# Performance work log

Measured on AMD Instinct MI355X. Metric: run time of the kernel, lower is better.

Reference implementation:

```python
import jax, jax.numpy as jnp
import numpy as np

N_MODES, BATCH, PH, PW = 4, 1024, 128, 128
OBJ_C, OBJ_H, OBJ_W = 1, 2048, 2048


def setup_inputs() -> dict:
    key = jax.random.key(0)
    k1, k2, k3 = jax.random.split(key, 3)
    obj = jax.random.normal(k1, (OBJ_C, OBJ_H, OBJ_W), dtype=jnp.float32)
    waves = jax.random.normal(k2, (N_MODES, BATCH, PH, PW), dtype=jnp.float32)
    pos = jax.random.randint(k3, (BATCH, 2), 0, OBJ_H - PH, dtype=jnp.int32)
    return {"obj": obj, "waves": waves, "pos": pos}


def reference(obj, waves, pos):
    B, H, W = waves.shape[1], waves.shape[2], waves.shape[3]
    # patch_norm = sum over probe modes of |waves|^2  -> [B, H, W]
    patch_norm = jnp.sum(waves * waves, axis=0)
    # overlap_intensity: scatter-add each patch into object_norm at its corner pos
    rows = pos[:, 0, None] + jnp.arange(H)          # [B, H]
    cols = pos[:, 1, None] + jnp.arange(W)          # [B, W]
    object_norm = jnp.zeros(obj.shape[1:], jnp.float32).at[
        rows[:, :, None], cols[:, None, :]
    ].add(patch_norm)
    # batch_crop: gather object patches at each position -> [B, C, H, W]
    C = obj.shape[0]
    def crop_one(p):
        return jax.lax.dynamic_slice(obj, (0, p[0], p[1]), (C, H, W))
    patches = jax.vmap(crop_one)(pos)
    return patches, object_norm
```

## Files before the change

kernel.cpp:

```cpp
#include <hip/hip_runtime.h>


#define NMODES 4
#define NB     1024
#define PH     128
#define PW     128
#define OH     2048
#define OW     2048

#define TS       32
#define NT_X     (OW / TS)
#define NT_Y     (OH / TS)
#define NT       (NT_X * NT_Y)
#define CAP      64
#define UNROLL   4

__global__ __launch_bounds__(256) void crop_and_bin(
    const float* __restrict__ obj,
    const int*   __restrict__ pos,
    float* __restrict__ patches,
    int*   __restrict__ tile_cnt,
    int*   __restrict__ tile_list)
{
    const int q = blockIdx.x * blockDim.x + threadIdx.x;

    if (q < NB) {
        const int r0 = pos[2 * q];
        const int c0 = pos[2 * q + 1];
        const int ty0 = r0 >> 5, ty1 = (r0 + PH - 1) >> 5;
        const int tx0 = c0 >> 5, tx1 = (c0 + PW - 1) >> 5;
        for (int ty = ty0; ty <= ty1; ++ty)
            for (int tx = tx0; tx <= tx1; ++tx) {
                const int t = ty * NT_X + tx;
                const int idx = atomicAdd(&tile_cnt[t], 1);
                if (idx < CAP) tile_list[t * CAP + idx] = q;
            }
    }

    const int b     = q >> 12;
    const int local = q & 4095;
    const int h     = local >> 5;
    const int w     = (local & 31) << 2;

    const int r0 = pos[b * 2 + 0];
    const int c0 = pos[b * 2 + 1];

    const int oidx = (r0 + h) * OW + (c0 + w);
    float4 p;
    p.x = obj[oidx + 0];
    p.y = obj[oidx + 1];
    p.z = obj[oidx + 2];
    p.w = obj[oidx + 3];
    *reinterpret_cast<float4*>(patches + b * (PH * PW) + h * PW + w) = p;
}

__global__ __launch_bounds__(256) void norm_gather(
    const float* __restrict__ waves,
    const int*   __restrict__ pos,
    const int*   __restrict__ tile_cnt,
    const int*   __restrict__ tile_list,
    float* __restrict__ norm)
{
    const int t  = blockIdx.x;
    const int Y0 = (t >> 6) * TS;
    const int X0 = (t & 63) * TS;

    __shared__ int s_base[CAP + UNROLL];
    __shared__ int s_r[CAP + UNROLL];
    __shared__ int s_c[CAP + UNROLL];

    const int count = min(tile_cnt[t], CAP);
    const int cpad  = (count + UNROLL - 1) & ~(UNROLL - 1);
    for (int i = threadIdx.x; i < cpad; i += 256) {
        if (i < count) {
            const int b = tile_list[t * CAP + i];
            s_base[i] = b * (PH * PW);
            s_r[i]    = pos[2 * b];
            s_c[i]    = pos[2 * b + 1];
        } else {
            s_base[i] = 0;
            s_r[i]    = 1 << 20;
            s_c[i]    = 1 << 20;
        }
    }
    __syncthreads();

    const int x     = threadIdx.x & 31;
    const int phase = threadIdx.x >> 5;
    const int X     = X0 + x;
    const int Y     = Y0 + phase;

    const int MS = NB * PH * PW;

    float acc0 = 0.0f, acc1 = 0.0f, acc2 = 0.0f, acc3 = 0.0f;

    #pragma unroll 2
    for (int i = 0; i < cpad; ++i) {
        const int r0 = s_r[i];
        const int c0 = s_c[i];
        const int bb = s_base[i];

        const int dc  = X - c0;
        const bool vc = (unsigned)dc < (unsigned)PW;
        const int dcc = min(max(dc, 0), PW - 1);

        const int dr0 = Y      - r0;
        const int dr1 = Y + 8  - r0;
        const int dr2 = Y + 16 - r0;
        const int dr3 = Y + 24 - r0;

        const bool v0 = vc & ((unsigned)dr0 < (unsigned)PH);
        const bool v1 = vc & ((unsigned)dr1 < (unsigned)PH);
        const bool v2 = vc & ((unsigned)dr2 < (unsigned)PH);
        const bool v3 = vc & ((unsigned)dr3 < (unsigned)PH);

        const int drc0 = min(max(dr0, 0), PH - 1);
        const int drc1 = min(max(dr1, 0), PH - 1);
        const int drc2 = min(max(dr2, 0), PH - 1);
        const int drc3 = min(max(dr3, 0), PH - 1);

        const float* w0p = waves + bb + drc0 * PW + dcc;
        const float* w1p = waves + bb + drc1 * PW + dcc;
        const float* w2p = waves + bb + drc2 * PW + dcc;
        const float* w3p = waves + bb + drc3 * PW + dcc;

        const float a0 = w0p[0], a1 = w0p[MS], a2 = w0p[2 * MS], a3 = w0p[3 * MS];
        const float b0 = w1p[0], b1 = w1p[MS], b2 = w1p[2 * MS], b3 = w1p[3 * MS];
        const float c0f = w2p[0], c1 = w2p[MS], c2 = w2p[2 * MS], c3 = w2p[3 * MS];
        const float d0 = w3p[0], d1 = w3p[MS], d2 = w3p[2 * MS], d3 = w3p[3 * MS];

        const float s0 = a0 * a0 + a1 * a1 + a2 * a2 + a3 * a3;
        const float s1 = b0 * b0 + b1 * b1 + b2 * b2 + b3 * b3;
        const float s2 = c0f * c0f + c1 * c1 + c2 * c2 + c3 * c3;
        const float s3 = d0 * d0 + d1 * d1 + d2 * d2 + d3 * d3;

        acc0 += v0 ? s0 : 0.0f;
        acc1 += v1 ? s1 : 0.0f;
        acc2 += v2 ? s2 : 0.0f;
        acc3 += v3 ? s3 : 0.0f;
    }

    norm[(Y     ) * OW + X] = acc0;
    norm[(Y +  8) * OW + X] = acc1;
    norm[(Y + 16) * OW + X] = acc2;
    norm[(Y + 24) * OW + X] = acc3;
}

extern "C" void kernel_launch(void* const* d_in, const int* in_sizes, int n_in,
                              void* d_out, int out_size, void* d_ws, size_t ws_size,
                              hipStream_t stream) {
    const float* obj   = (const float*)d_in[0];
    const float* waves = (const float*)d_in[1];
    const int*   pos   = (const int*)d_in[2];

    float* patches = (float*)d_out;
    float* norm    = (float*)d_out + (size_t)NB * PH * PW;

    int* tile_cnt  = (int*)d_ws;
    int* tile_list = tile_cnt + NT;

    hipMemsetAsync(tile_cnt, 0, NT * sizeof(int), stream);

    const int quads = NB * PH * PW / 4;
    crop_and_bin<<<quads / 256, 256, 0, stream>>>(obj, pos, patches,
                                                  tile_cnt, tile_list);
    norm_gather<<<NT, 256, 0, stream>>>(waves, pos, tile_cnt,
                                        tile_list, norm);
}
```

Before: 430.1 us.

## Use 128-wide bins sliced into 8-row blocks with row-overlap skip

Enlarges the binning tiles from 32x32 to 128x128, which cuts the per-patch atomic bin insertions from up to 25 to up to 4. Each bin is now processed by 16 blocks of 8 rows by 128 columns, so each warp reads full 128-float patch rows. Each block skips patches whose rows do not overlap its slice. Each block scans a longer candidate list, and lanes outside a patch's columns still issue clamped loads. The CAP of 64 per bin is more likely to overflow with larger tiles.

```diff
diff --git a/kernel.cpp b/kernel.cpp
--- a/kernel.cpp
+++ b/kernel.cpp
@@ -8,12 +8,13 @@
 #define OH     2048
 #define OW     2048
 
-#define TS       32
+#define TS       128
 #define NT_X     (OW / TS)
 #define NT_Y     (OH / TS)
 #define NT       (NT_X * NT_Y)
 #define CAP      64
-#define UNROLL   4
+#define SLICES   16
+#define SH       (TS / SLICES)
 
 __global__ __launch_bounds__(256) void crop_and_bin(
     const float* __restrict__ obj,
@@ -27,8 +28,8 @@
     if (q < NB) {
         const int r0 = pos[2 * q];
         const int c0 = pos[2 * q + 1];
-        const int ty0 = r0 >> 5, ty1 = (r0 + PH - 1) >> 5;
-        const int tx0 = c0 >> 5, tx1 = (c0 + PW - 1) >> 5;
+        const int ty0 = r0 >> 7, ty1 = (r0 + PH - 1) >> 7;
+        const int tx0 = c0 >> 7, tx1 = (c0 + PW - 1) >> 7;
         for (int ty = ty0; ty <= ty1; ++ty)
             for (int tx = tx0; tx <= tx1; ++tx) {
                 const int t = ty * NT_X + tx;
@@ -61,32 +62,27 @@
     const int*   __restrict__ tile_list,
     float* __restrict__ norm)
 {
-    const int t  = blockIdx.x;
-    const int Y0 = (t >> 6) * TS;
-    const int X0 = (t & 63) * TS;
+    const int blk = blockIdx.x;
+    const int t   = blk >> 4;
+    const int s   = blk & 15;
+    const int Y0  = (t >> 4) * TS + s * SH;
+    const int X0  = (t & 15) * TS;
 
-    __shared__ int s_base[CAP + UNROLL];
-    __shared__ int s_r[CAP + UNROLL];
-    __shared__ int s_c[CAP + UNROLL];
+    __shared__ int s_base[CAP];
+    __shared__ int s_r[CAP];
+    __shared__ int s_c[CAP];
 
     const int count = min(tile_cnt[t], CAP);
-    const int cpad  = (count + UNROLL - 1) & ~(UNROLL - 1);
-    for (int i = threadIdx.x; i < cpad; i += 256) {
-        if (i < count) {
-            const int b = tile_list[t * CAP + i];
-            s_base[i] = b * (PH * PW);
-            s_r[i]    = pos[2 * b];
-            s_c[i]    = pos[2 * b + 1];
-        } else {
-            s_base[i] = 0;
-            s_r[i]    = 1 << 20;
-            s_c[i]    = 1 << 20;
-        }
+    for (int i = threadIdx.x; i < count; i += 256) {
+        const int b = tile_list[t * CAP + i];
+        s_base[i] = b * (PH * PW);
+        s_r[i]    = pos[2 * b];
+        s_c[i]    = pos[2 * b + 1];
     }
     __syncthreads();
 
-    const int x     = threadIdx.x & 31;
-    const int phase = threadIdx.x >> 5;
+    const int x     = threadIdx.x & 127;
+    const int phase = threadIdx.x >> 7;
     const int X     = X0 + x;
     const int Y     = Y0 + phase;
 
@@ -94,44 +90,41 @@
 
     float acc0 = 0.0f, acc1 = 0.0f, acc2 = 0.0f, acc3 = 0.0f;
 
-    #pragma unroll 2
-    for (int i = 0; i < cpad; ++i) {
+    for (int i = 0; i < count; ++i) {
         const int r0 = s_r[i];
+        if (r0 >= Y0 + SH || r0 + PH <= Y0) continue;
+
         const int c0 = s_c[i];
         const int bb = s_base[i];
 
         const int dc  = X - c0;
         const bool vc = (unsigned)dc < (unsigned)PW;
         const int dcc = min(max(dc, 0), PW - 1);
+        const float* wp = waves + bb + dcc;
 
-        const int dr0 = Y      - r0;
-        const int dr1 = Y + 8  - r0;
-        const int dr2 = Y + 16 - r0;
-        const int dr3 = Y + 24 - r0;
+        const int dr0 = Y     - r0;
+        const int dr1 = dr0 + 2;
+        const int dr2 = dr0 + 4;
+        const int dr3 = dr0 + 6;
 
         const bool v0 = vc & ((unsigned)dr0 < (unsigned)PH);
         const bool v1 = vc & ((unsigned)dr1 < (unsigned)PH);
         const bool v2 = vc & ((unsigned)dr2 < (unsigned)PH);
         const bool v3 = vc & ((unsigned)dr3 < (unsigned)PH);
 
-        const int drc0 = min(max(dr0, 0), PH - 1);
-        const int drc1 = min(max(dr1, 0), PH - 1);
-        const int drc2 = min(max(dr2, 0), PH - 1);
-        const int drc3 = min(max(dr3, 0), PH - 1);
+        const int o0 = min(max(dr0, 0), PH - 1) * PW;
+        const int o1 = min(max(dr1, 0), PH - 1) * PW;
+        const int o2 = min(max(dr2, 0), PH - 1) * PW;
+        const int o3 = min(max(dr3, 0), PH - 1) * PW;
 
-        const float* w0p = waves + bb + drc0 * PW + dcc;
-        const float* w1p = waves + bb + drc1 * PW + dcc;
-        const float* w2p = waves + bb + drc2 * PW + dcc;
-        const float* w3p = waves + bb + drc3 * PW + dcc;
-
-        const float a0 = w0p[0], a1 = w0p[MS], a2 = w0p[2 * MS], a3 = w0p[3 * MS];
-        const float b0 = w1p[0], b1 = w1p[MS], b2 = w1p[2 * MS], b3 = w1p[3 * MS];
-        const float c0f = w2p[0], c1 = w2p[MS], c2 = w2p[2 * MS], c3 = w2p[3 * MS];
-        const float d0 = w3p[0], d1 = w3p[MS], d2 = w3p[2 * MS], d3 = w3p[3 * MS];
+        const float a0 = wp[o0], a1 = wp[o0 + MS], a2 = wp[o0 + 2 * MS], a3 = wp[o0 + 3 * MS];
+        const float b0 = wp[o1], b1 = wp[o1 + MS], b2 = wp[o1 + 2 * MS], b3 = wp[o1 + 3 * MS];
+        const float e0 = wp[o2], e1 = wp[o2 + MS], e2 = wp[o2 + 2 * MS], e3 = wp[o2 + 3 * MS];
+        const float d0 = wp[o3], d1 = wp[o3 + MS], d2 = wp[o3 + 2 * MS], d3 = wp[o3 + 3 * MS];
 
         const float s0 = a0 * a0 + a1 * a1 + a2 * a2 + a3 * a3;
         const float s1 = b0 * b0 + b1 * b1 + b2 * b2 + b3 * b3;
-        const float s2 = c0f * c0f + c1 * c1 + c2 * c2 + c3 * c3;
+        const float s2 = e0 * e0 + e1 * e1 + e2 * e2 + e3 * e3;
         const float s3 = d0 * d0 + d1 * d1 + d2 * d2 + d3 * d3;
 
         acc0 += v0 ? s0 : 0.0f;
@@ -140,10 +133,10 @@
         acc3 += v3 ? s3 : 0.0f;
     }
 
-    norm[(Y     ) * OW + X] = acc0;
-    norm[(Y +  8) * OW + X] = acc1;
-    norm[(Y + 16) * OW + X] = acc2;
-    norm[(Y + 24) * OW + X] = acc3;
+    norm[(Y    ) * OW + X] = acc0;
+    norm[(Y + 2) * OW + X] = acc1;
+    norm[(Y + 4) * OW + X] = acc2;
+    norm[(Y + 6) * OW + X] = acc3;
 }
 
 extern "C" void kernel_launch(void* const* d_in, const int* in_sizes, int n_in,
@@ -159,11 +152,11 @@
     int* tile_cnt  = (int*)d_ws;
     int* tile_list = tile_cnt + NT;
 
-    hipMemsetAsync(tile_cnt, 0, NT * sizeof(int), stream);
+    (void)hipMemsetAsync(tile_cnt, 0, NT * sizeof(int), stream);
 
     const int quads = NB * PH * PW / 4;
     crop_and_bin<<<quads / 256, 256, 0, stream>>>(obj, pos, patches,
                                                   tile_cnt, tile_list);
-    norm_gather<<<NT, 256, 0, stream>>>(waves, pos, tile_cnt,
-                                        tile_list, norm);
+    norm_gather<<<NT * SLICES, 256, 0, stream>>>(waves, pos, tile_cnt,
+                                                 tile_list, norm);
 }
```

New measurement: 416.2 us. 3.2% less time.
